# Kernel tuning notes

Measured on AMD Instinct MI355X. Metric: run time of the kernel, lower is better.

The kernel has to match this reference:

```python
import jax, jax.numpy as jnp
import numpy as np

N = 262144   # total atoms/nodes in the batch
F = 128      # node feature dim
G = 4096     # number of graphs (segments)
H = 512      # n_hidden
T = 3        # set2set recurrent steps


def hard_sigmoid(x):
    return jnp.clip(0.2 * x + 0.5, 0.0, 1.0)


def setup_inputs() -> dict:
    key = jax.random.key(0)
    k1, k2, k3, k4 = jax.random.split(key, 4)
    features = jax.random.normal(k1, (1, N, F), dtype=jnp.float32)
    weights = jax.random.uniform(k2, (1, N), dtype=jnp.float32)
    # sorted graph ids, every segment non-empty (TF segment_* need sorted ids)
    index = ((jnp.arange(N) * G) // N).astype(jnp.int32).reshape(1, N)
    m_weight = jax.random.normal(k3, (F, H), dtype=jnp.float32) * 0.05
    m_bias = jnp.zeros((H,), dtype=jnp.float32)
    recurrent_kernel = jax.random.normal(k4, (2 * H, 4 * H), dtype=jnp.float32) * 0.02
    # unit_forget_bias: [zeros(H), ones(H), zeros(2H)]
    recurrent_bias = jnp.concatenate(
        [jnp.zeros((H,)), jnp.ones((H,)), jnp.zeros((2 * H,))]).astype(jnp.float32)
    return {
        "features": features,
        "weights": weights,
        "index": index,
        "m_weight": m_weight,
        "m_bias": m_bias,
        "recurrent_kernel": recurrent_kernel,
        "recurrent_bias": recurrent_bias,
    }


def reference(features, weights, index, m_weight, m_bias,
              recurrent_kernel, recurrent_bias):
    idx = index.reshape(-1)                       # [N]
    m = features @ m_weight + m_bias              # [1, N, H]
    c = jnp.zeros((1, G, H), dtype=features.dtype)
    q_star = jnp.zeros((1, G, 2 * H), dtype=features.dtype)
    for _ in range(T):
        # LSTM cell on q_star
        z = q_star @ recurrent_kernel + recurrent_bias   # [1, G, 4H]
        zi, zf, zc, zo = jnp.split(z, 4, axis=-1)
        i = hard_sigmoid(zi)
        f = hard_sigmoid(zf)
        c = f * c + i * jnp.tanh(zc)
        h = hard_sigmoid(zo) * jnp.tanh(c)               # [1, G, H]
        # per-node attention logits
        h_nodes = h[:, idx, :]                           # [1, N, H] gather
        e = jnp.sum(m * h_nodes, axis=-1)                # [1, N]
        maxes = jax.ops.segment_max(e[0], idx, num_segments=G,
                                    indices_are_sorted=True)
        e = e - maxes[idx][None, :]
        ex = jnp.exp(e) * weights                        # weighted softmax numerator
        seg_sum = jax.ops.segment_sum(ex[0], idx, num_segments=G,
                                      indices_are_sorted=True)
        a = ex / seg_sum[idx][None, :]                   # [1, N]
        r = jax.ops.segment_sum((m * a[..., None])[0], idx, num_segments=G,
                                indices_are_sorted=True)[None]  # [1, G, H]
        q_star = jnp.concatenate([h, r], axis=-1)        # [1, G, 2H]
    return q_star
```

## Files before the change

kernel.cpp:

```cpp
#include <hip/hip_runtime.h>
#include <cstddef>

#define NN 262144
#define F_DIM 128
#define G_SEG 4096
#define H_DIM 512
#define SEG_SZ 64
#define KDIM 1024
#define NDIM 2048

typedef unsigned short u16;
typedef __attribute__((ext_vector_type(8))) __bf16 bf16x8;
typedef __attribute__((ext_vector_type(4))) float f32x4;

__device__ __forceinline__ float hsig(float x) {
    return fminf(fmaxf(0.2f * x + 0.5f, 0.0f), 1.0f);
}

__device__ __forceinline__ u16 f2bf(float x) {
    union { float f; unsigned u; } v; v.f = x;
    unsigned r = (v.u + 0x7fffu + ((v.u >> 16) & 1u)) >> 16;
    return (u16)r;
}

__global__ void k_transpose(const float* __restrict__ mw, float* __restrict__ mwT) {
    int id = blockIdx.x * blockDim.x + threadIdx.x;
    if (id < F_DIM * H_DIM) {
        int f = id / H_DIM, j = id % H_DIM;
        mwT[j * F_DIM + f] = mw[id];
    }
}

__global__ __launch_bounds__(256) void k_bt(const float* __restrict__ rk, u16* __restrict__ btg) {
    __shared__ u16 t[64][65];
    int tid = threadIdx.x;
    int n0 = blockIdx.x * 64, k0 = blockIdx.y * 64;
    for (int i = tid; i < 64 * 64; i += 256) {
        int r = i >> 6, cc = i & 63;
        t[r][cc] = f2bf(rk[(size_t)(k0 + r) * NDIM + n0 + cc]);
    }
    __syncthreads();
    for (int i = tid; i < 64 * 64; i += 256) {
        int n = i >> 6, k = i & 63;
        int nc = n0 + n;
        int q = nc >> 9, jj = nc & 511;
        int rn = (jj >> 5) * 128 + q * 32 + (jj & 31);
        btg[(size_t)rn * KDIM + k0 + k] = t[k][n];
    }
}

#define GBM 128
#define GBK 32
__global__ __launch_bounds__(256) void k_gemm_gates(const u16* __restrict__ A,
                                                    const u16* __restrict__ BTG,
                                                    const float* __restrict__ rb,
                                                    float* __restrict__ c,
                                                    float* __restrict__ out,
                                                    u16* __restrict__ qsb) {
    __shared__ u16 sA[GBM * GBK];
    __shared__ u16 sB[GBM * GBK];
    int tid = threadIdx.x;
    int lane = tid & 63, wv = tid >> 6;
    int wm = wv * 32;
    int bm = blockIdx.y * GBM;
    int j0 = blockIdx.x * 32;
    const u16* Ab = A + (size_t)bm * KDIM;
    const u16* Bb = BTG + (size_t)(blockIdx.x * 128) * KDIM;
    int r16 = lane & 15, kc = lane >> 4;
    f32x4 acc[2][8] = {};

    for (int k0 = 0; k0 < KDIM; k0 += GBK) {
#pragma unroll
        for (int i = 0; i < 2; ++i) {
            int ch = i * 256 + tid;
            int row = ch >> 2, cc = ch & 3;
            int ccs = cc ^ ((row >> 1) & 3);
            __builtin_amdgcn_global_load_lds(
                (const __attribute__((address_space(1))) void*)(Ab + (size_t)row * KDIM + k0 + ccs * 8),
                (__attribute__((address_space(3))) void*)(&sA[ch * 8]), 16, 0, 0);
            __builtin_amdgcn_global_load_lds(
                (const __attribute__((address_space(1))) void*)(Bb + (size_t)row * KDIM + k0 + ccs * 8),
                (__attribute__((address_space(3))) void*)(&sB[ch * 8]), 16, 0, 0);
        }
        __syncthreads();
        bf16x8 af[2], bfr[8];
#pragma unroll
        for (int mi = 0; mi < 2; ++mi) {
            int row = wm + mi * 16 + r16;
            int off = row * GBK + ((kc ^ ((row >> 1) & 3)) * 8);
            af[mi] = *reinterpret_cast<const bf16x8*>(&sA[off]);
        }
#pragma unroll
        for (int ni = 0; ni < 8; ++ni) {
            int row = ni * 16 + r16;
            int off = row * GBK + ((kc ^ ((row >> 1) & 3)) * 8);
            bfr[ni] = *reinterpret_cast<const bf16x8*>(&sB[off]);
        }
#pragma unroll
        for (int mi = 0; mi < 2; ++mi)
#pragma unroll
            for (int ni = 0; ni < 8; ++ni)
                acc[mi][ni] = __builtin_amdgcn_mfma_f32_16x16x32_bf16(af[mi], bfr[ni], acc[mi][ni], 0, 0, 0);
        __syncthreads();
    }

    float rbv[4][2];
#pragma unroll
    for (int q = 0; q < 4; ++q) {
        rbv[q][0] = rb[q * H_DIM + j0 + r16];
        rbv[q][1] = rb[q * H_DIM + j0 + 16 + r16];
    }
#pragma unroll
    for (int mi = 0; mi < 2; ++mi)
#pragma unroll
        for (int r = 0; r < 4; ++r) {
            int row = bm + wm + mi * 16 + kc * 4 + r;
#pragma unroll
            for (int jj = 0; jj < 2; ++jj) {
                int j = j0 + jj * 16 + r16;
                float zi = acc[mi][0 + jj][r] + rbv[0][jj];
                float zf = acc[mi][2 + jj][r] + rbv[1][jj];
                float zc = acc[mi][4 + jj][r] + rbv[2][jj];
                float zo = acc[mi][6 + jj][r] + rbv[3][jj];
                size_t ci = (size_t)row * H_DIM + j;
                float cn = hsig(zf) * c[ci] + hsig(zi) * tanhf(zc);
                c[ci] = cn;
                float h = hsig(zo) * tanhf(cn);
                out[(size_t)row * 1024 + j] = h;
                qsb[(size_t)row * 1024 + j] = f2bf(h);
            }
        }
}

__global__ void k_gates0(const float* __restrict__ rb,
                         float* __restrict__ c, float* __restrict__ out,
                         u16* __restrict__ qsb) {
    int id = blockIdx.x * blockDim.x + threadIdx.x;
    int g = id >> 9, j = id & 511;
    float zi = rb[j], zc = rb[2 * H_DIM + j], zo = rb[3 * H_DIM + j];
    float cn = hsig(zi) * tanhf(zc);
    c[id] = cn;
    float h = hsig(zo) * tanhf(cn);
    out[(size_t)g * 1024 + j] = h;
    qsb[(size_t)g * 1024 + j] = f2bf(h);
}

#define WSEG 16
#define WBK 128
__global__ __launch_bounds__(256) void k_W(const float* __restrict__ out,
                                           const float* __restrict__ mwT,
                                           const float* __restrict__ mb,
                                           float* __restrict__ W,
                                           float* __restrict__ bsum) {
    __shared__ float smw[WBK][F_DIM];
    __shared__ float shl[WSEG][WBK];
    int g0 = blockIdx.x * WSEG;
    int t = threadIdx.x;
    int f = t & 127, sh = t >> 7;
    float acc[8] = {};
    for (int k0 = 0; k0 < H_DIM; k0 += WBK) {
        for (int i = t; i < WBK * 32; i += 256) {
            int r = i >> 5, c4 = (i & 31) << 2;
            *reinterpret_cast<float4*>(&smw[r][c4]) =
                *reinterpret_cast<const float4*>(&mwT[(size_t)(k0 + r) * F_DIM + c4]);
        }
        for (int i = t; i < WSEG * WBK / 4; i += 256) {
            int s = i >> 5, c4 = (i & 31) << 2;
            *reinterpret_cast<float4*>(&shl[s][c4]) =
                *reinterpret_cast<const float4*>(&out[(size_t)(g0 + s) * 1024 + k0 + c4]);
        }
        __syncthreads();
        for (int kk = 0; kk < WBK; ++kk) {
            float w = smw[kk][f];
#pragma unroll
            for (int s = 0; s < 8; ++s)
                acc[s] = fmaf(shl[sh + 2 * s][kk], w, acc[s]);
        }
        __syncthreads();
    }
#pragma unroll
    for (int s = 0; s < 8; ++s)
        W[(size_t)(g0 + sh + 2 * s) * F_DIM + f] = acc[s];
    int wv = t >> 6, lane = t & 63;
    for (int si = 0; si < 4; ++si) {
        int g = g0 + wv + si * 4;
        float b = 0.f;
        for (int j = lane; j < H_DIM; j += 64)
            b = fmaf(out[(size_t)g * 1024 + j], mb[j], b);
#pragma unroll
        for (int off = 32; off >= 1; off >>= 1) b += __shfl_xor(b, off);
        if (lane == 0) bsum[g] = b;
    }
}

__global__ __launch_bounds__(128) void k_attn(const float* __restrict__ feats,
                                              const float* __restrict__ wts,
                                              const float* __restrict__ W,
                                              const float* __restrict__ bsum,
                                              float* __restrict__ fsum) {
    int g = blockIdx.x;
    int t = threadIdx.x;
    __shared__ float fl[SEG_SZ * 129];
    __shared__ float Wl[F_DIM];
    __shared__ float ep[2][SEG_SZ];
    __shared__ float al[SEG_SZ];
    const float4* f4 = reinterpret_cast<const float4*>(feats + (size_t)g * SEG_SZ * F_DIM);
    for (int i = t; i < SEG_SZ * F_DIM / 4; i += 128) {
        float4 v = f4[i];
        int n = i >> 5;
        int f = (i & 31) << 2;
        float* p = &fl[n * 129 + f];
        p[0] = v.x; p[1] = v.y; p[2] = v.z; p[3] = v.w;
    }
    Wl[t] = W[g * F_DIM + t];
    __syncthreads();
    int row = t & 63, half = t >> 6;
    const float* fr = &fl[row * 129 + half * 64];
    const float* wr = &Wl[half * 64];
    float e = 0.f;
#pragma unroll
    for (int f = 0; f < 64; ++f) e = fmaf(fr[f], wr[f], e);
    ep[half][row] = e;
    __syncthreads();
    if (t < 64) {
        float ee = ep[0][t] + ep[1][t] + bsum[g];
        float mx = ee;
#pragma unroll
        for (int off = 32; off >= 1; off >>= 1) mx = fmaxf(mx, __shfl_xor(mx, off));
        float ex = expf(ee - mx) * wts[g * SEG_SZ + t];
        float s = ex;
#pragma unroll
        for (int off = 32; off >= 1; off >>= 1) s += __shfl_xor(s, off);
        al[t] = ex / s;
    }
    __syncthreads();
    float a0 = 0.f;
#pragma unroll
    for (int n = 0; n < SEG_SZ; ++n)
        a0 = fmaf(al[n], fl[n * 129 + t], a0);
    fsum[g * F_DIM + t] = a0;
}

#define RGB 8
__global__ __launch_bounds__(512) void k_r(const float* __restrict__ fsum,
                                           const float* __restrict__ mw,
                                           const float* __restrict__ mb,
                                           float* __restrict__ out,
                                           u16* __restrict__ qsb) {
    int g0 = blockIdx.x * RGB;
    int tid = threadIdx.x;
    __shared__ float fs[RGB][F_DIM];
    for (int i = tid; i < RGB * F_DIM; i += 512)
        fs[i >> 7][i & 127] = fsum[g0 * F_DIM + i];
    __syncthreads();
    float acc[RGB] = {};
    for (int f = 0; f < F_DIM; ++f) {
        float w = mw[f * H_DIM + tid];
#pragma unroll
        for (int s = 0; s < RGB; ++s) acc[s] = fmaf(fs[s][f], w, acc[s]);
    }
    float bias = mb[tid];
#pragma unroll
    for (int s = 0; s < RGB; ++s) {
        float v = acc[s] + bias;
        out[(size_t)(g0 + s) * 1024 + H_DIM + tid] = v;
        qsb[(size_t)(g0 + s) * 1024 + H_DIM + tid] = f2bf(v);
    }
}

extern "C" void kernel_launch(void* const* d_in, const int* in_sizes, int n_in,
                              void* d_out, int out_size, void* d_ws, size_t ws_size,
                              hipStream_t stream) {
    const float* feats = (const float*)d_in[0];
    const float* wts   = (const float*)d_in[1];
    const float* mw    = (const float*)d_in[3];
    const float* mb    = (const float*)d_in[4];
    const float* rk    = (const float*)d_in[5];
    const float* rb    = (const float*)d_in[6];
    float* out = (float*)d_out;

    float* c    = (float*)d_ws;
    float* W    = c + (size_t)G_SEG * H_DIM;
    float* bs   = W + (size_t)G_SEG * F_DIM;
    float* fsum = bs + G_SEG;
    float* mwT  = fsum + (size_t)G_SEG * F_DIM;
    u16*   qsb  = (u16*)(mwT + H_DIM * F_DIM);
    u16*   btg  = qsb + (size_t)G_SEG * KDIM;

    k_transpose<<<(F_DIM * H_DIM + 255) / 256, 256, 0, stream>>>(mw, mwT);
    k_bt<<<dim3(NDIM / 64, KDIM / 64), 256, 0, stream>>>(rk, btg);

    for (int t = 0; t < 3; ++t) {
        if (t > 0) {
            k_gemm_gates<<<dim3(H_DIM / 32, G_SEG / GBM), 256, 0, stream>>>(qsb, btg, rb, c, out, qsb);
        } else {
            k_gates0<<<(G_SEG * H_DIM) / 256, 256, 0, stream>>>(rb, c, out, qsb);
        }
        k_W<<<G_SEG / WSEG, 256, 0, stream>>>(out, mwT, mb, W, bs);
        k_attn<<<G_SEG, 128, 0, stream>>>(feats, wts, W, bs, fsum);
        k_r<<<G_SEG / RGB, 512, 0, stream>>>(fsum, mw, mb, out, qsb);
    }
}
```

Before: 521.3 us.

## Fold m_weight into recurrent kernel to shrink gate GEMM K and skip r projection

Precomputes M2 = m_weight @ recurrent_kernel[512:] and a folded bias, so the gate GEMM consumes [h, fsum] with K=640 instead of [h, r] with K=1024. The r projection kernel now runs only on the last step, and the attention kernel writes bf16 fsum straight into the GEMM input. At t=0, where h is identical for every graph, k_W runs a single block and k_attn broadcasts its result. This cuts GEMM work and the per-step r projection, at the cost of extra one-time precompute kernels and a different rounding order, since M2 is rounded to bf16.

```diff
diff --git a/kernel.cpp b/kernel.cpp
--- a/kernel.cpp
+++ b/kernel.cpp
@@ -8,6 +8,7 @@
 #define SEG_SZ 64
 #define KDIM 1024
 #define NDIM 2048
+#define KA 640
 
 typedef unsigned short u16;
 typedef __attribute__((ext_vector_type(8))) __bf16 bf16x8;
@@ -31,7 +32,12 @@
     }
 }
 
-__global__ __launch_bounds__(256) void k_bt(const float* __restrict__ rk, u16* __restrict__ btg) {
+__device__ __forceinline__ int permrow(int n) {
+    int q = n >> 9, jj = n & 511;
+    return (jj >> 5) * 128 + q * 32 + (jj & 31);
+}
+
+__global__ __launch_bounds__(256) void k_bt(const float* __restrict__ rk, u16* __restrict__ btg2) {
     __shared__ u16 t[64][65];
     int tid = threadIdx.x;
     int n0 = blockIdx.x * 64, k0 = blockIdx.y * 64;
@@ -42,21 +48,62 @@
     __syncthreads();
     for (int i = tid; i < 64 * 64; i += 256) {
         int n = i >> 6, k = i & 63;
-        int nc = n0 + n;
-        int q = nc >> 9, jj = nc & 511;
-        int rn = (jj >> 5) * 128 + q * 32 + (jj & 31);
-        btg[(size_t)rn * KDIM + k0 + k] = t[k][n];
-    }
+        btg2[(size_t)permrow(n0 + n) * KA + k0 + k] = t[k][n];
+    }
+}
+
+__global__ __launch_bounds__(256) void k_M2(const float* __restrict__ rk,
+                                            const float* __restrict__ mwT,
+                                            u16* __restrict__ btg2) {
+    __shared__ float srk[64][64];
+    __shared__ float smw[64][128];
+    int n0 = blockIdx.x * 64;
+    int t = threadIdx.x;
+    int f = t & 127, nh = t >> 7;
+    float acc[32] = {};
+    for (int k0 = 0; k0 < H_DIM; k0 += 64) {
+        for (int i = t; i < 64 * 64; i += 256) {
+            int kk = i >> 6, nn = i & 63;
+            srk[kk][nn] = rk[(size_t)(512 + k0 + kk) * NDIM + n0 + nn];
+        }
+        for (int i = t; i < 64 * 128; i += 256) {
+            int ff = i & 127, kk = i >> 7;
+            smw[kk][ff] = mwT[(size_t)(k0 + kk) * F_DIM + ff];
+        }
+        __syncthreads();
+        for (int kk = 0; kk < 64; ++kk) {
+            float w = smw[kk][f];
+#pragma unroll
+            for (int s = 0; s < 32; ++s)
+                acc[s] = fmaf(w, srk[kk][nh * 32 + s], acc[s]);
+        }
+        __syncthreads();
+    }
+    for (int s = 0; s < 32; ++s) {
+        int n = n0 + nh * 32 + s;
+        btg2[(size_t)permrow(n) * KA + 512 + f] = f2bf(acc[s]);
+    }
+}
+
+__global__ __launch_bounds__(256) void k_rb2(const float* __restrict__ rk,
+                                             const float* __restrict__ rb,
+                                             const float* __restrict__ mb,
+                                             float* __restrict__ rb2) {
+    int n = blockIdx.x * 256 + threadIdx.x;
+    float acc = rb[n];
+    for (int j = 0; j < H_DIM; ++j)
+        acc = fmaf(mb[j], rk[(size_t)(512 + j) * NDIM + n], acc);
+    rb2[n] = acc;
 }
 
 #define GBM 128
 #define GBK 32
 __global__ __launch_bounds__(256) void k_gemm_gates(const u16* __restrict__ A,
                                                     const u16* __restrict__ BTG,
-                                                    const float* __restrict__ rb,
+                                                    const float* __restrict__ rb2,
                                                     float* __restrict__ c,
                                                     float* __restrict__ out,
-                                                    u16* __restrict__ qsb) {
+                                                    u16* __restrict__ qsa) {
     __shared__ u16 sA[GBM * GBK];
     __shared__ u16 sB[GBM * GBK];
     int tid = threadIdx.x;
@@ -64,22 +111,22 @@
     int wm = wv * 32;
     int bm = blockIdx.y * GBM;
     int j0 = blockIdx.x * 32;
-    const u16* Ab = A + (size_t)bm * KDIM;
-    const u16* Bb = BTG + (size_t)(blockIdx.x * 128) * KDIM;
+    const u16* Ab = A + (size_t)bm * KA;
+    const u16* Bb = BTG + (size_t)(blockIdx.x * 128) * KA;
     int r16 = lane & 15, kc = lane >> 4;
     f32x4 acc[2][8] = {};
 
-    for (int k0 = 0; k0 < KDIM; k0 += GBK) {
+    for (int k0 = 0; k0 < KA; k0 += GBK) {
 #pragma unroll
         for (int i = 0; i < 2; ++i) {
             int ch = i * 256 + tid;
             int row = ch >> 2, cc = ch & 3;
             int ccs = cc ^ ((row >> 1) & 3);
             __builtin_amdgcn_global_load_lds(
-                (const __attribute__((address_space(1))) void*)(Ab + (size_t)row * KDIM + k0 + ccs * 8),
+                (const __attribute__((address_space(1))) void*)(Ab + (size_t)row * KA + k0 + ccs * 8),
                 (__attribute__((address_space(3))) void*)(&sA[ch * 8]), 16, 0, 0);
             __builtin_amdgcn_global_load_lds(
-                (const __attribute__((address_space(1))) void*)(Bb + (size_t)row * KDIM + k0 + ccs * 8),
+                (const __attribute__((address_space(1))) void*)(Bb + (size_t)row * KA + k0 + ccs * 8),
                 (__attribute__((address_space(3))) void*)(&sB[ch * 8]), 16, 0, 0);
         }
         __syncthreads();
@@ -107,8 +154,8 @@
     float rbv[4][2];
 #pragma unroll
     for (int q = 0; q < 4; ++q) {
-        rbv[q][0] = rb[q * H_DIM + j0 + r16];
-        rbv[q][1] = rb[q * H_DIM + j0 + 16 + r16];
+        rbv[q][0] = rb2[q * H_DIM + j0 + r16];
+        rbv[q][1] = rb2[q * H_DIM + j0 + 16 + r16];
     }
 #pragma unroll
     for (int mi = 0; mi < 2; ++mi)
@@ -127,14 +174,14 @@
                 c[ci] = cn;
                 float h = hsig(zo) * tanhf(cn);
                 out[(size_t)row * 1024 + j] = h;
-                qsb[(size_t)row * 1024 + j] = f2bf(h);
+                qsa[(size_t)row * KA + j] = f2bf(h);
             }
         }
 }
 
 __global__ void k_gates0(const float* __restrict__ rb,
                          float* __restrict__ c, float* __restrict__ out,
-                         u16* __restrict__ qsb) {
+                         u16* __restrict__ qsa) {
     int id = blockIdx.x * blockDim.x + threadIdx.x;
     int g = id >> 9, j = id & 511;
     float zi = rb[j], zc = rb[2 * H_DIM + j], zo = rb[3 * H_DIM + j];
@@ -142,54 +189,61 @@
     c[id] = cn;
     float h = hsig(zo) * tanhf(cn);
     out[(size_t)g * 1024 + j] = h;
-    qsb[(size_t)g * 1024 + j] = f2bf(h);
+    qsa[(size_t)g * KA + j] = f2bf(h);
 }
 
 #define WSEG 16
-#define WBK 128
 __global__ __launch_bounds__(256) void k_W(const float* __restrict__ out,
                                            const float* __restrict__ mwT,
                                            const float* __restrict__ mb,
                                            float* __restrict__ W,
                                            float* __restrict__ bsum) {
-    __shared__ float smw[WBK][F_DIM];
-    __shared__ float shl[WSEG][WBK];
+    __shared__ float smw[128][F_DIM];
+    __shared__ float shl[WSEG][128];
+    __shared__ float smb[128];
+    __shared__ float bacc[WSEG][16];
     int g0 = blockIdx.x * WSEG;
     int t = threadIdx.x;
     int f = t & 127, sh = t >> 7;
+    bacc[t >> 4][t & 15] = 0.f;
     float acc[8] = {};
-    for (int k0 = 0; k0 < H_DIM; k0 += WBK) {
-        for (int i = t; i < WBK * 32; i += 256) {
+    for (int k0 = 0; k0 < H_DIM; k0 += 128) {
+        for (int i = t; i < 128 * 32; i += 256) {
             int r = i >> 5, c4 = (i & 31) << 2;
             *reinterpret_cast<float4*>(&smw[r][c4]) =
                 *reinterpret_cast<const float4*>(&mwT[(size_t)(k0 + r) * F_DIM + c4]);
         }
-        for (int i = t; i < WSEG * WBK / 4; i += 256) {
+        for (int i = t; i < WSEG * 32; i += 256) {
             int s = i >> 5, c4 = (i & 31) << 2;
             *reinterpret_cast<float4*>(&shl[s][c4]) =
                 *reinterpret_cast<const float4*>(&out[(size_t)(g0 + s) * 1024 + k0 + c4]);
         }
-        __syncthreads();
-        for (int kk = 0; kk < WBK; ++kk) {
+        if (t < 128) smb[t] = mb[k0 + t];
+        __syncthreads();
+        for (int kk = 0; kk < 128; ++kk) {
             float w = smw[kk][f];
 #pragma unroll
             for (int s = 0; s < 8; ++s)
                 acc[s] = fmaf(shl[sh + 2 * s][kk], w, acc[s]);
         }
+        {
+            int s = t >> 4, l16 = t & 15;
+            float pb = 0.f;
+#pragma unroll
+            for (int m = 0; m < 8; ++m)
+                pb = fmaf(shl[s][l16 * 8 + m], smb[l16 * 8 + m], pb);
+            bacc[s][l16] += pb;
+        }
         __syncthreads();
     }
 #pragma unroll
     for (int s = 0; s < 8; ++s)
         W[(size_t)(g0 + sh + 2 * s) * F_DIM + f] = acc[s];
-    int wv = t >> 6, lane = t & 63;
-    for (int si = 0; si < 4; ++si) {
-        int g = g0 + wv + si * 4;
+    if (t < WSEG) {
         float b = 0.f;
-        for (int j = lane; j < H_DIM; j += 64)
-            b = fmaf(out[(size_t)g * 1024 + j], mb[j], b);
-#pragma unroll
-        for (int off = 32; off >= 1; off >>= 1) b += __shfl_xor(b, off);
-        if (lane == 0) bsum[g] = b;
+#pragma unroll
+        for (int i = 0; i < 16; ++i) b += bacc[t][i];
+        bsum[g0 + t] = b;
     }
 }
 
@@ -197,7 +251,9 @@
                                               const float* __restrict__ wts,
                                               const float* __restrict__ W,
                                               const float* __restrict__ bsum,
-                                              float* __restrict__ fsum) {
+                                              float* __restrict__ fsum,
+                                              u16* __restrict__ qsa,
+                                              int gmul) {
     int g = blockIdx.x;
     int t = threadIdx.x;
     __shared__ float fl[SEG_SZ * 129];
@@ -212,7 +268,7 @@
         float* p = &fl[n * 129 + f];
         p[0] = v.x; p[1] = v.y; p[2] = v.z; p[3] = v.w;
     }
-    Wl[t] = W[g * F_DIM + t];
+    Wl[t] = W[(size_t)(g * gmul) * F_DIM + t];
     __syncthreads();
     int row = t & 63, half = t >> 6;
     const float* fr = &fl[row * 129 + half * 64];
@@ -223,7 +279,7 @@
     ep[half][row] = e;
     __syncthreads();
     if (t < 64) {
-        float ee = ep[0][t] + ep[1][t] + bsum[g];
+        float ee = ep[0][t] + ep[1][t] + bsum[g * gmul];
         float mx = ee;
 #pragma unroll
         for (int off = 32; off >= 1; off >>= 1) mx = fmaxf(mx, __shfl_xor(mx, off));
@@ -239,14 +295,14 @@
     for (int n = 0; n < SEG_SZ; ++n)
         a0 = fmaf(al[n], fl[n * 129 + t], a0);
     fsum[g * F_DIM + t] = a0;
+    qsa[(size_t)g * KA + 512 + t] = f2bf(a0);
 }
 
 #define RGB 8
 __global__ __launch_bounds__(512) void k_r(const float* __restrict__ fsum,
                                            const float* __restrict__ mw,
                                            const float* __restrict__ mb,
-                                           float* __restrict__ out,
-                                           u16* __restrict__ qsb) {
+                                           float* __restrict__ out) {
     int g0 = blockIdx.x * RGB;
     int tid = threadIdx.x;
     __shared__ float fs[RGB][F_DIM];
@@ -261,11 +317,8 @@
     }
     float bias = mb[tid];
 #pragma unroll
-    for (int s = 0; s < RGB; ++s) {
-        float v = acc[s] + bias;
-        out[(size_t)(g0 + s) * 1024 + H_DIM + tid] = v;
-        qsb[(size_t)(g0 + s) * 1024 + H_DIM + tid] = f2bf(v);
-    }
+    for (int s = 0; s < RGB; ++s)
+        out[(size_t)(g0 + s) * 1024 + H_DIM + tid] = acc[s] + bias;
 }
 
 extern "C" void kernel_launch(void* const* d_in, const int* in_sizes, int n_in,
@@ -284,20 +337,24 @@
     float* bs   = W + (size_t)G_SEG * F_DIM;
     float* fsum = bs + G_SEG;
     float* mwT  = fsum + (size_t)G_SEG * F_DIM;
-    u16*   qsb  = (u16*)(mwT + H_DIM * F_DIM);
-    u16*   btg  = qsb + (size_t)G_SEG * KDIM;
+    float* rb2  = mwT + (size_t)H_DIM * F_DIM;
+    u16*   qsa  = (u16*)(rb2 + NDIM);
+    u16*   btg2 = qsa + (size_t)G_SEG * KA;
 
     k_transpose<<<(F_DIM * H_DIM + 255) / 256, 256, 0, stream>>>(mw, mwT);
-    k_bt<<<dim3(NDIM / 64, KDIM / 64), 256, 0, stream>>>(rk, btg);
+    k_bt<<<dim3(NDIM / 64, 512 / 64), 256, 0, stream>>>(rk, btg2);
+    k_M2<<<NDIM / 64, 256, 0, stream>>>(rk, mwT, btg2);
+    k_rb2<<<NDIM / 256, 256, 0, stream>>>(rk, rb, mb, rb2);
 
     for (int t = 0; t < 3; ++t) {
         if (t > 0) {
-            k_gemm_gates<<<dim3(H_DIM / 32, G_SEG / GBM), 256, 0, stream>>>(qsb, btg, rb, c, out, qsb);
+            k_gemm_gates<<<dim3(H_DIM / 32, G_SEG / GBM), 256, 0, stream>>>(qsa, btg2, rb2, c, out, qsa);
         } else {
-            k_gates0<<<(G_SEG * H_DIM) / 256, 256, 0, stream>>>(rb, c, out, qsb);
-        }
-        k_W<<<G_SEG / WSEG, 256, 0, stream>>>(out, mwT, mb, W, bs);
-        k_attn<<<G_SEG, 128, 0, stream>>>(feats, wts, W, bs, fsum);
-        k_r<<<G_SEG / RGB, 512, 0, stream>>>(fsum, mw, mb, out, qsb);
-    }
-}
+            k_gates0<<<(G_SEG * H_DIM) / 256, 256, 0, stream>>>(rb, c, out, qsa);
+        }
+        k_W<<<(t == 0) ? 1 : (G_SEG / WSEG), 256, 0, stream>>>(out, mwT, mb, W, bs);
+        k_attn<<<G_SEG, 128, 0, stream>>>(feats, wts, W, bs, fsum, qsa, (t == 0) ? 0 : 1);
+        if (t == 2)
+            k_r<<<G_SEG / RGB, 512, 0, stream>>>(fsum, mw, mb, out);
+    }
+}
```

New measurement: 551.4 us. +5.8%, slower.
